# Kernel optimization log

Hardware: AMD Instinct MI355X
Metric: run time of the kernel (lower is better)

Reference implementation:

```python
import jax, jax.numpy as jnp
import numpy as np

N, E = 50000, 800000
IN, H = 128, 128
NTYPE, NSCHOOL, NTIME, NAUTHOR = 20, 30, 15, 200


def setup_inputs() -> dict:
    key = jax.random.key(0)
    ks = jax.random.split(key, 20)

    def lin(k, i, o):  # kaiming-ish init
        return jax.random.normal(k, (i, o), jnp.float32) * (1.0 / np.sqrt(i))

    return {
        "x0": jax.random.normal(ks[0], (N, IN), jnp.float32),
        "edge_index": jax.random.randint(ks[1], (2, E), 0, N, dtype=jnp.int64),
        # GCNConv weights (x @ W + b after aggregation)
        "W1": lin(ks[2], IN, H),   "b1": jnp.zeros((H,), jnp.float32),
        "Wt": lin(ks[3], H, NTYPE),    "bt": jnp.zeros((NTYPE,), jnp.float32),
        "Ws": lin(ks[4], H, NSCHOOL), "bs": jnp.zeros((NSCHOOL,), jnp.float32),
        "Wa": lin(ks[5], H, NAUTHOR), "ba": jnp.zeros((NAUTHOR,), jnp.float32),
        # classification heads (Linear stored as [in, out])
        "Wct": lin(ks[6], NTYPE, NTYPE),       "bct": jnp.zeros((NTYPE,), jnp.float32),
        "Wcs": lin(ks[7], NSCHOOL, NSCHOOL), "bcs": jnp.zeros((NSCHOOL,), jnp.float32),
        "Wtf": lin(ks[8], IN, NTIME),          "btf": jnp.zeros((NTIME,), jnp.float32),
        "Wca": lin(ks[9], NAUTHOR, NAUTHOR), "bca": jnp.zeros((NAUTHOR,), jnp.float32),
    }


def reference(x0, edge_index, W1, b1, Wt, bt, Ws, bs, Wa, ba,
              Wct, bct, Wcs, bcs, Wtf, btf, Wca, bca):
    n = x0.shape[0]
    src, dst = edge_index[0], edge_index[1]
    # GCNConv default: add self-loops, symmetric deg^{-1/2} normalization
    loop = jnp.arange(n, dtype=edge_index.dtype)
    src_f = jnp.concatenate([src, loop])  # [E+N]
    dst_f = jnp.concatenate([dst, loop])
    deg = jax.ops.segment_sum(jnp.ones(src_f.shape[0], jnp.float32), dst_f, num_segments=n)
    dinv = jnp.where(deg > 0, jax.lax.rsqrt(deg), 0.0)
    norm = dinv[src_f] * dinv[dst_f]  # [E+N]

    def conv(x, W, b):
        xt = x @ W                                   # transform first (small out dim)
        msg = xt[src_f] * norm[:, None]              # [E+N, out]
        return jax.ops.segment_sum(msg, dst_f, num_segments=n) + b

    h = jax.nn.relu(conv(x0, W1, b1))  # dropout is identity at inference

    out_type = jax.nn.softmax(conv(h, Wt, bt) @ Wct + bct, axis=-1)
    out_school = jax.nn.softmax(conv(h, Ws, bs) @ Wcs + bcs, axis=-1)
    out_time = jax.nn.softmax(x0 @ Wtf + btf, axis=-1)  # head reads x0 directly
    out_author = jax.nn.softmax(conv(h, Wa, ba) @ Wca + bca, axis=-1)
    return (out_type, out_school, out_time, out_author)
```

## Files before the change

kernel.cpp:

```cpp
#include <hip/hip_runtime.h>
#include <math.h>


typedef short short8 __attribute__((ext_vector_type(8)));
typedef float f32x4 __attribute__((ext_vector_type(4)));

static __device__ __forceinline__ unsigned short f2bf(float x) {
  unsigned u = __float_as_uint(x);
  u += 0x7fff + ((u >> 16) & 1);
  return (unsigned short)(u >> 16);
}
static __device__ __forceinline__ unsigned pack2bf(float lo, float hi) {
  return ((unsigned)f2bf(hi) << 16) | (unsigned)f2bf(lo);
}
static __device__ __forceinline__ float bflo(unsigned u) {
  return __uint_as_float(u << 16);
}
static __device__ __forceinline__ float bfhi(unsigned u) {
  return __uint_as_float(u & 0xffff0000u);
}

__global__ void k_zero(int* __restrict__ p, int n) {
  int i = blockIdx.x * blockDim.x + threadIdx.x;
  if (i < n) p[i] = 0;
}

__global__ void k_deg(const int* __restrict__ dst, int E, int* __restrict__ deg) {
  int e = blockIdx.x * blockDim.x + threadIdx.x;
  if (e < E) atomicAdd(&deg[dst[e]], 1);
}

__global__ void k_scan1(const int* __restrict__ deg, int n,
                        int* __restrict__ excl, int* __restrict__ bsum) {
  __shared__ int sm[256];
  int i = blockIdx.x * 256 + threadIdx.x;
  int v = (i < n) ? deg[i] : 0;
  sm[threadIdx.x] = v;
  __syncthreads();
#pragma unroll
  for (int o = 1; o < 256; o <<= 1) {
    int t = (threadIdx.x >= o) ? sm[threadIdx.x - o] : 0;
    __syncthreads();
    sm[threadIdx.x] += t;
    __syncthreads();
  }
  if (i < n) excl[i] = sm[threadIdx.x] - v;
  if (threadIdx.x == 255) bsum[blockIdx.x] = sm[255];
}

__global__ void k_scan2(int* __restrict__ bsum, int nb) {
  __shared__ int sm[256];
  int v = (threadIdx.x < nb) ? bsum[threadIdx.x] : 0;
  sm[threadIdx.x] = v;
  __syncthreads();
#pragma unroll
  for (int o = 1; o < 256; o <<= 1) {
    int t = (threadIdx.x >= o) ? sm[threadIdx.x - o] : 0;
    __syncthreads();
    sm[threadIdx.x] += t;
    __syncthreads();
  }
  if (threadIdx.x < nb) bsum[threadIdx.x] = sm[threadIdx.x] - v;
}

__global__ void k_finalize(int* __restrict__ row_off, const int* __restrict__ bsum,
                           const int* __restrict__ deg, int* __restrict__ cursor,
                           float* __restrict__ dinv, int n) {
  int i = blockIdx.x * 256 + threadIdx.x;
  if (i < n) {
    int ro = row_off[i] + bsum[blockIdx.x];
    row_off[i] = ro;
    cursor[i] = ro;
    dinv[i] = rsqrtf((float)(deg[i] + 1));
  }
}

__global__ void k_fill(const int* __restrict__ src, const int* __restrict__ dst,
                       int E, int* __restrict__ cursor, int* __restrict__ csr) {
  int e = blockIdx.x * blockDim.x + threadIdx.x;
  if (e < E) {
    int d = dst[e];
    int p = atomicAdd(&cursor[d], 1);
    csr[p] = src[e];
  }
}

__global__ __launch_bounds__(256) void k_scale(
    const float* __restrict__ X, const float* __restrict__ dinv,
    unsigned* __restrict__ Y, int n) {
  int t = blockIdx.x * 256 + threadIdx.x;
  int total = n * 64;
  if (t < total) {
    int row = t >> 6;
    float d = dinv[row];
    float2 v = reinterpret_cast<const float2*>(X)[t];
    Y[t] = pack2bf(v.x * d, v.y * d);
  }
}

__global__ __launch_bounds__(256) void k_agg(
    const unsigned* __restrict__ Y, unsigned* __restrict__ out,
    const int* __restrict__ row_off, const int* __restrict__ deg,
    const int* __restrict__ csr, const float* __restrict__ dinv, int n) {
  int wave = threadIdx.x >> 6;
  int lane = threadIdx.x & 63;
  int i = blockIdx.x * 4 + wave;
  if (i >= n) return;
  int start = row_off[i];
  int cnt = deg[i];
  float ax = 0.f, ay = 0.f;
  int j = 0;
  for (; j + 3 < cnt; j += 4) {
    int s0 = csr[start + j];
    int s1 = csr[start + j + 1];
    int s2 = csr[start + j + 2];
    int s3 = csr[start + j + 3];
    unsigned u0 = Y[(size_t)s0 * 64 + lane];
    unsigned u1 = Y[(size_t)s1 * 64 + lane];
    unsigned u2 = Y[(size_t)s2 * 64 + lane];
    unsigned u3 = Y[(size_t)s3 * 64 + lane];
    ax += (bflo(u0) + bflo(u1)) + (bflo(u2) + bflo(u3));
    ay += (bfhi(u0) + bfhi(u1)) + (bfhi(u2) + bfhi(u3));
  }
  for (; j < cnt; ++j) {
    int s0 = csr[start + j];
    unsigned u0 = Y[(size_t)s0 * 64 + lane];
    ax += bflo(u0);
    ay += bfhi(u0);
  }
  unsigned us = Y[(size_t)i * 64 + lane];
  float di = dinv[i];
  out[(size_t)i * 64 + lane] = pack2bf((ax + bflo(us)) * di, (ay + bfhi(us)) * di);
}

__global__ void k_pack128(const float* __restrict__ W, unsigned short* __restrict__ P) {
  int t = blockIdx.x * 256 + threadIdx.x;
  int i = t >> 7, c = t & 127;
  P[((i >> 3) * 128 + c) * 8 + (i & 7)] = f2bf(W[t]);
}

__global__ void k_fuse(const float* __restrict__ Wt, const float* __restrict__ bt,
                       const float* __restrict__ Wct, const float* __restrict__ bct,
                       const float* __restrict__ Ws, const float* __restrict__ bs,
                       const float* __restrict__ Wcs, const float* __restrict__ bcs,
                       const float* __restrict__ Wa, const float* __restrict__ ba,
                       const float* __restrict__ Wca, const float* __restrict__ bca,
                       unsigned short* __restrict__ WfPk, float* __restrict__ bf) {
  int c = blockIdx.x;
  int i = threadIdx.x;
  float acc = 0.f, bacc = 0.f;
  if (c < 20) {
    for (int k = 0; k < 20; ++k) {
      float w2 = Wct[k * 20 + c];
      acc += Wt[i * 20 + k] * w2;
      bacc += bt[k] * w2;
    }
    bacc += bct[c];
  } else if (c < 50) {
    int cc = c - 20;
    for (int k = 0; k < 30; ++k) {
      float w2 = Wcs[k * 30 + cc];
      acc += Ws[i * 30 + k] * w2;
      bacc += bs[k] * w2;
    }
    bacc += bcs[cc];
  } else if (c < 250) {
    int cc = c - 50;
    for (int k = 0; k < 200; ++k) {
      float w2 = Wca[k * 200 + cc];
      acc += Wa[i * 200 + k] * w2;
      bacc += ba[k] * w2;
    }
    bacc += bca[cc];
  }
  WfPk[((i >> 3) * 256 + c) * 8 + (i & 7)] = f2bf(acc);
  if (i == 0) bf[c] = bacc;
}

__global__ __launch_bounds__(256) void k_mfma_gemm128(
    const short* __restrict__ A, const unsigned short* __restrict__ Wpk,
    const float* __restrict__ bias, const float* __restrict__ dinv,
    unsigned short* __restrict__ out, int n) {
  int wave = threadIdx.x >> 6, lane = threadIdx.x & 63;
  int lr = lane & 15, lg = lane >> 4;
  int r0 = blockIdx.x * 64 + wave * 16;
  if (r0 >= n) return;
  int ar = r0 + lr;
  if (ar >= n) ar = n - 1;
  const short* Arow = A + (size_t)ar * 128;
  short8 afr[4];
#pragma unroll
  for (int kk = 0; kk < 4; ++kk)
    afr[kk] = *reinterpret_cast<const short8*>(Arow + kk * 32 + lg * 8);
  f32x4 acc[8];
#pragma unroll
  for (int t = 0; t < 8; ++t) acc[t] = (f32x4){0.f, 0.f, 0.f, 0.f};
  const short8* Wp8 = reinterpret_cast<const short8*>(Wpk);
#pragma unroll
  for (int t = 0; t < 8; ++t) {
#pragma unroll
    for (int kk = 0; kk < 4; ++kk) {
      short8 bfr = Wp8[(kk * 4 + lg) * 128 + t * 16 + lr];
      acc[t] = __builtin_amdgcn_mfma_f32_16x16x32_bf16(afr[kk], bfr, acc[t], 0, 0, 0);
    }
  }
  int rloc = r0 + lg * 4;
#pragma unroll
  for (int t = 0; t < 8; ++t) {
    int col = t * 16 + lr;
    float b = bias[col];
#pragma unroll
    for (int reg = 0; reg < 4; ++reg) {
      int row = rloc + reg;
      if (row < n) {
        float v = fmaxf(acc[t][reg] + b, 0.f) * dinv[row];
        out[(size_t)row * 128 + col] = f2bf(v);
      }
    }
  }
}

__global__ __launch_bounds__(256) void k_heads_fused(
    const short* __restrict__ A, const unsigned short* __restrict__ Wpk,
    const float* __restrict__ bf, float* __restrict__ outT,
    float* __restrict__ outS, float* __restrict__ outA, int n) {
  int wave = threadIdx.x >> 6, lane = threadIdx.x & 63;
  int lr = lane & 15, lg = lane >> 4;
  int r0 = blockIdx.x * 64 + wave * 16;
  if (r0 >= n) return;
  int ar = r0 + lr;
  if (ar >= n) ar = n - 1;
  const short* Arow = A + (size_t)ar * 128;
  short8 afr[4];
#pragma unroll
  for (int kk = 0; kk < 4; ++kk)
    afr[kk] = *reinterpret_cast<const short8*>(Arow + kk * 32 + lg * 8);
  f32x4 acc[16];
#pragma unroll
  for (int t = 0; t < 16; ++t) acc[t] = (f32x4){0.f, 0.f, 0.f, 0.f};
  const short8* Wp8 = reinterpret_cast<const short8*>(Wpk);
#pragma unroll
  for (int t = 0; t < 16; ++t) {
#pragma unroll
    for (int kk = 0; kk < 4; ++kk) {
      short8 bfr = Wp8[(kk * 4 + lg) * 256 + t * 16 + lr];
      acc[t] = __builtin_amdgcn_mfma_f32_16x16x32_bf16(afr[kk], bfr, acc[t], 0, 0, 0);
    }
  }
  float bias_l[16];
#pragma unroll
  for (int t = 0; t < 16; ++t) bias_l[t] = bf[t * 16 + lr];
  int rloc = r0 + lg * 4;
#pragma unroll
  for (int reg = 0; reg < 4; ++reg) {
    int row = rloc + reg;
    float v[16];
    float mT = -INFINITY, mS = -INFINITY, mA = -INFINITY;
#pragma unroll
    for (int t = 0; t < 16; ++t) {
      v[t] = acc[t][reg] + bias_l[t];
      int c = t * 16 + lr;
      if (c < 20) mT = fmaxf(mT, v[t]);
      else if (c < 50) mS = fmaxf(mS, v[t]);
      else if (c < 250) mA = fmaxf(mA, v[t]);
    }
#pragma unroll
    for (int o = 8; o; o >>= 1) {
      mT = fmaxf(mT, __shfl_xor(mT, o, 64));
      mS = fmaxf(mS, __shfl_xor(mS, o, 64));
      mA = fmaxf(mA, __shfl_xor(mA, o, 64));
    }
    float sT = 0.f, sS = 0.f, sA = 0.f;
#pragma unroll
    for (int t = 0; t < 16; ++t) {
      int c = t * 16 + lr;
      float m = (c < 20) ? mT : (c < 50) ? mS : mA;
      float ex = __expf(v[t] - m);
      v[t] = ex;
      if (c < 20) sT += ex;
      else if (c < 50) sS += ex;
      else if (c < 250) sA += ex;
    }
#pragma unroll
    for (int o = 8; o; o >>= 1) {
      sT += __shfl_xor(sT, o, 64);
      sS += __shfl_xor(sS, o, 64);
      sA += __shfl_xor(sA, o, 64);
    }
    float iT = 1.f / sT, iS = 1.f / sS, iA = 1.f / sA;
    if (row < n) {
#pragma unroll
      for (int t = 0; t < 16; ++t) {
        int c = t * 16 + lr;
        if (c < 20) outT[(size_t)row * 20 + c] = v[t] * iT;
        else if (c < 50) outS[(size_t)row * 30 + (c - 20)] = v[t] * iS;
        else if (c < 250) outA[(size_t)row * 200 + (c - 50)] = v[t] * iA;
      }
    }
  }
}

__global__ __launch_bounds__(256) void k_time(
    const float* __restrict__ x0, const float* __restrict__ Wtf,
    const float* __restrict__ btf, float* __restrict__ outT, int n) {
  __shared__ float sW[128][16];
  __shared__ float sb[16];
  for (int t = threadIdx.x; t < 128 * 16; t += 256) {
    int k = t >> 4, j = t & 15;
    sW[k][j] = (j < 15) ? Wtf[k * 15 + j] : 0.f;
  }
  if (threadIdx.x < 16) sb[threadIdx.x] = (threadIdx.x < 15) ? btf[threadIdx.x] : 0.f;
  __syncthreads();
  int j = threadIdx.x & 15;
  int rl = threadIdx.x >> 4;
  int r = blockIdx.x * 16 + rl;
  if (r >= n) return;
  float acc = sb[j];
  const float4* xr = reinterpret_cast<const float4*>(x0 + (size_t)r * 128);
  for (int k4 = 0; k4 < 32; ++k4) {
    float4 xv = xr[k4];
    acc += xv.x * sW[k4 * 4 + 0][j] + xv.y * sW[k4 * 4 + 1][j] +
           xv.z * sW[k4 * 4 + 2][j] + xv.w * sW[k4 * 4 + 3][j];
  }
  float m = (j < 15) ? acc : -INFINITY;
#pragma unroll
  for (int o = 8; o; o >>= 1) m = fmaxf(m, __shfl_xor(m, o, 16));
  float e = (j < 15) ? __expf(acc - m) : 0.f;
  float s = e;
#pragma unroll
  for (int o = 8; o; o >>= 1) s += __shfl_xor(s, o, 16);
  if (j < 15) outT[(size_t)r * 15 + j] = e / s;
}

extern "C" void kernel_launch(void* const* d_in, const int* in_sizes, int n_in,
                              void* d_out, int out_size, void* d_ws, size_t ws_size,
                              hipStream_t stream) {
  const float* x0 = (const float*)d_in[0];
  const int* ei = (const int*)d_in[1];
  const float* W1 = (const float*)d_in[2];
  const float* b1 = (const float*)d_in[3];
  const float* Wt = (const float*)d_in[4];
  const float* bt = (const float*)d_in[5];
  const float* Ws = (const float*)d_in[6];
  const float* bs = (const float*)d_in[7];
  const float* Wa = (const float*)d_in[8];
  const float* ba = (const float*)d_in[9];
  const float* Wct = (const float*)d_in[10];
  const float* bct = (const float*)d_in[11];
  const float* Wcs = (const float*)d_in[12];
  const float* bcs = (const float*)d_in[13];
  const float* Wtf = (const float*)d_in[14];
  const float* btf = (const float*)d_in[15];
  const float* Wca = (const float*)d_in[16];
  const float* bca = (const float*)d_in[17];
  (void)n_in; (void)out_size; (void)ws_size;

  int N = in_sizes[0] / 128;
  int E = in_sizes[1] / 2;
  float* out = (float*)d_out;

  char* ws = (char*)d_ws;
  size_t off = 0;
  auto alloc = [&](size_t bytes) -> void* {
    void* p = ws + off;
    off = (off + bytes + 255) & ~(size_t)255;
    return p;
  };
  int* deg = (int*)alloc((size_t)N * 4);
  int* row_off = (int*)alloc((size_t)N * 4);
  int* bsum = (int*)alloc(256 * 4);
  int* cursor = (int*)alloc((size_t)N * 4);
  float* dinv = (float*)alloc((size_t)N * 4);
  int* csr = (int*)alloc((size_t)E * 4);
  unsigned short* WfPk = (unsigned short*)alloc((size_t)128 * 256 * 2);
  unsigned short* W1Pk = (unsigned short*)alloc((size_t)128 * 128 * 2);
  float* bf = (float*)alloc(256 * 4);
  unsigned* Yb = (unsigned*)alloc((size_t)N * 64 * 4);
  unsigned* Ab = (unsigned*)alloc((size_t)N * 64 * 4);
  unsigned* Bb = (unsigned*)alloc((size_t)N * 64 * 4);

  const int* srcp = ei;
  const int* dstp = ei + E;
  int gE = (E + 255) / 256;
  int gN = (N + 255) / 256;

  k_zero<<<gN, 256, 0, stream>>>(deg, N);
  k_deg<<<gE, 256, 0, stream>>>(dstp, E, deg);
  k_scan1<<<gN, 256, 0, stream>>>(deg, N, row_off, bsum);
  k_scan2<<<1, 256, 0, stream>>>(bsum, gN);
  k_finalize<<<gN, 256, 0, stream>>>(row_off, bsum, deg, cursor, dinv, N);
  k_fill<<<gE, 256, 0, stream>>>(srcp, dstp, E, cursor, csr);
  k_pack128<<<64, 256, 0, stream>>>(W1, W1Pk);
  k_fuse<<<256, 128, 0, stream>>>(Wt, bt, Wct, bct, Ws, bs, Wcs, bcs, Wa, ba, Wca,
                                  bca, WfPk, bf);
  k_scale<<<(N * 64 + 255) / 256, 256, 0, stream>>>(x0, dinv, Yb, N);
  k_agg<<<(N + 3) / 4, 256, 0, stream>>>(Yb, Ab, row_off, deg, csr, dinv, N);
  k_mfma_gemm128<<<(N + 63) / 64, 256, 0, stream>>>(
      (const short*)Ab, W1Pk, b1, dinv, (unsigned short*)Bb, N);
  k_agg<<<(N + 3) / 4, 256, 0, stream>>>(Bb, Ab, row_off, deg, csr, dinv, N);
  k_heads_fused<<<(N + 63) / 64, 256, 0, stream>>>(
      (const short*)Ab, WfPk, bf, out, out + (size_t)N * 20, out + (size_t)N * 65, N);
  k_time<<<(N + 15) / 16, 256, 0, stream>>>(x0, Wtf, btf, out + (size_t)N * 50, N);
}
```

Measured before the change: 381.6 us.

## Split GEMM and heads columns across wave pairs with LDS-staged A tiles

Both MFMA kernels now handle 32 rows per block. The A tile is staged through shared memory, and each pair of waves splits the output columns between them, so twice as many blocks launch and each wave holds half the accumulators. In the fused heads kernel the author softmax spans both column halves, so row max and row sum are exchanged through LDS with extra barriers. This aims to raise occupancy and parallelism, at the cost of more blocks, extra syncs, and each block reading the weight matrix for its share of the columns.

```diff
diff --git a/kernel.cpp b/kernel.cpp
--- a/kernel.cpp
+++ b/kernel.cpp
@@ -177,37 +177,49 @@
   if (i == 0) bf[c] = bacc;
 }
 
+static __device__ __forceinline__ void stage32(
+    const short* __restrict__ A, short (*sAb)[136], int rowBase, int n, int tid) {
+  for (int t = tid; t < 32 * 16; t += 256) {
+    int r = t >> 4, c8 = t & 15;
+    int gr = rowBase + r;
+    short8 v = (short8){0, 0, 0, 0, 0, 0, 0, 0};
+    if (gr < n) v = *reinterpret_cast<const short8*>(A + (size_t)gr * 128 + c8 * 8);
+    *reinterpret_cast<short8*>(&sAb[r][c8 * 8]) = v;
+  }
+}
+
 __global__ __launch_bounds__(256) void k_mfma_gemm128(
     const short* __restrict__ A, const unsigned short* __restrict__ Wpk,
     const float* __restrict__ bias, const float* __restrict__ dinv,
     unsigned short* __restrict__ out, int n) {
+  __shared__ short sAb[32][136];
+  int rowBase = blockIdx.x * 32;
+  stage32(A, sAb, rowBase, n, threadIdx.x);
+  __syncthreads();
   int wave = threadIdx.x >> 6, lane = threadIdx.x & 63;
+  int rg = wave >> 1, ch = wave & 1;
   int lr = lane & 15, lg = lane >> 4;
-  int r0 = blockIdx.x * 64 + wave * 16;
-  if (r0 >= n) return;
-  int ar = r0 + lr;
-  if (ar >= n) ar = n - 1;
-  const short* Arow = A + (size_t)ar * 128;
+  int r0 = rowBase + rg * 16;
   short8 afr[4];
 #pragma unroll
   for (int kk = 0; kk < 4; ++kk)
-    afr[kk] = *reinterpret_cast<const short8*>(Arow + kk * 32 + lg * 8);
-  f32x4 acc[8];
-#pragma unroll
-  for (int t = 0; t < 8; ++t) acc[t] = (f32x4){0.f, 0.f, 0.f, 0.f};
+    afr[kk] = *reinterpret_cast<const short8*>(&sAb[rg * 16 + lr][kk * 32 + lg * 8]);
+  f32x4 acc[4];
+#pragma unroll
+  for (int t = 0; t < 4; ++t) acc[t] = (f32x4){0.f, 0.f, 0.f, 0.f};
   const short8* Wp8 = reinterpret_cast<const short8*>(Wpk);
 #pragma unroll
-  for (int t = 0; t < 8; ++t) {
+  for (int t = 0; t < 4; ++t) {
 #pragma unroll
     for (int kk = 0; kk < 4; ++kk) {
-      short8 bfr = Wp8[(kk * 4 + lg) * 128 + t * 16 + lr];
+      short8 bfr = Wp8[(kk * 4 + lg) * 128 + ch * 64 + t * 16 + lr];
       acc[t] = __builtin_amdgcn_mfma_f32_16x16x32_bf16(afr[kk], bfr, acc[t], 0, 0, 0);
     }
   }
   int rloc = r0 + lg * 4;
 #pragma unroll
-  for (int t = 0; t < 8; ++t) {
-    int col = t * 16 + lr;
+  for (int t = 0; t < 4; ++t) {
+    int col = ch * 64 + t * 16 + lr;
     float b = bias[col];
 #pragma unroll
     for (int reg = 0; reg < 4; ++reg) {
@@ -224,45 +236,48 @@
     const short* __restrict__ A, const unsigned short* __restrict__ Wpk,
     const float* __restrict__ bf, float* __restrict__ outT,
     float* __restrict__ outS, float* __restrict__ outA, int n) {
+  __shared__ short sAb[32][136];
+  __shared__ float aM[2][2][16];
+  __shared__ float aS[2][2][16];
+  int rowBase = blockIdx.x * 32;
+  stage32(A, sAb, rowBase, n, threadIdx.x);
+  __syncthreads();
   int wave = threadIdx.x >> 6, lane = threadIdx.x & 63;
+  int rg = wave >> 1, ch = wave & 1;
   int lr = lane & 15, lg = lane >> 4;
-  int r0 = blockIdx.x * 64 + wave * 16;
-  if (r0 >= n) return;
-  int ar = r0 + lr;
-  if (ar >= n) ar = n - 1;
-  const short* Arow = A + (size_t)ar * 128;
+  int r0 = rowBase + rg * 16;
+  int cb = ch * 128;
   short8 afr[4];
 #pragma unroll
   for (int kk = 0; kk < 4; ++kk)
-    afr[kk] = *reinterpret_cast<const short8*>(Arow + kk * 32 + lg * 8);
-  f32x4 acc[16];
-#pragma unroll
-  for (int t = 0; t < 16; ++t) acc[t] = (f32x4){0.f, 0.f, 0.f, 0.f};
+    afr[kk] = *reinterpret_cast<const short8*>(&sAb[rg * 16 + lr][kk * 32 + lg * 8]);
+  f32x4 acc[8];
+#pragma unroll
+  for (int t = 0; t < 8; ++t) acc[t] = (f32x4){0.f, 0.f, 0.f, 0.f};
   const short8* Wp8 = reinterpret_cast<const short8*>(Wpk);
 #pragma unroll
-  for (int t = 0; t < 16; ++t) {
+  for (int t = 0; t < 8; ++t) {
 #pragma unroll
     for (int kk = 0; kk < 4; ++kk) {
-      short8 bfr = Wp8[(kk * 4 + lg) * 256 + t * 16 + lr];
+      short8 bfr = Wp8[(kk * 4 + lg) * 256 + cb + t * 16 + lr];
       acc[t] = __builtin_amdgcn_mfma_f32_16x16x32_bf16(afr[kk], bfr, acc[t], 0, 0, 0);
     }
   }
-  float bias_l[16];
-#pragma unroll
-  for (int t = 0; t < 16; ++t) bias_l[t] = bf[t * 16 + lr];
-  int rloc = r0 + lg * 4;
+  float bias_l[8];
+#pragma unroll
+  for (int t = 0; t < 8; ++t) bias_l[t] = bf[cb + t * 16 + lr];
+  float mTr[4], mSr[4], mAr[4];
 #pragma unroll
   for (int reg = 0; reg < 4; ++reg) {
-    int row = rloc + reg;
-    float v[16];
     float mT = -INFINITY, mS = -INFINITY, mA = -INFINITY;
 #pragma unroll
-    for (int t = 0; t < 16; ++t) {
-      v[t] = acc[t][reg] + bias_l[t];
-      int c = t * 16 + lr;
-      if (c < 20) mT = fmaxf(mT, v[t]);
-      else if (c < 50) mS = fmaxf(mS, v[t]);
-      else if (c < 250) mA = fmaxf(mA, v[t]);
+    for (int t = 0; t < 8; ++t) {
+      int c = cb + t * 16 + lr;
+      float val = acc[t][reg] + bias_l[t];
+      acc[t][reg] = val;
+      if (c < 20) mT = fmaxf(mT, val);
+      else if (c < 50) mS = fmaxf(mS, val);
+      else if (c < 250) mA = fmaxf(mA, val);
     }
 #pragma unroll
     for (int o = 8; o; o >>= 1) {
@@ -270,16 +285,26 @@
       mS = fmaxf(mS, __shfl_xor(mS, o, 64));
       mA = fmaxf(mA, __shfl_xor(mA, o, 64));
     }
+    mTr[reg] = mT; mSr[reg] = mS; mAr[reg] = mA;
+    if (lr == 0) aM[rg][ch][lg * 4 + reg] = mA;
+  }
+  __syncthreads();
+#pragma unroll
+  for (int reg = 0; reg < 4; ++reg)
+    mAr[reg] = fmaxf(mAr[reg], aM[rg][ch ^ 1][lg * 4 + reg]);
+  float sTr[4], sSr[4], sAr[4];
+#pragma unroll
+  for (int reg = 0; reg < 4; ++reg) {
     float sT = 0.f, sS = 0.f, sA = 0.f;
 #pragma unroll
-    for (int t = 0; t < 16; ++t) {
-      int c = t * 16 + lr;
-      float m = (c < 20) ? mT : (c < 50) ? mS : mA;
-      float ex = __expf(v[t] - m);
-      v[t] = ex;
-      if (c < 20) sT += ex;
-      else if (c < 50) sS += ex;
-      else if (c < 250) sA += ex;
+    for (int t = 0; t < 8; ++t) {
+      int c = cb + t * 16 + lr;
+      float m = (c < 20) ? mTr[reg] : (c < 50) ? mSr[reg] : mAr[reg];
+      float e = __expf(acc[t][reg] - m);
+      acc[t][reg] = e;
+      if (c < 20) sT += e;
+      else if (c < 50) sS += e;
+      else if (c < 250) sA += e;
     }
 #pragma unroll
     for (int o = 8; o; o >>= 1) {
@@ -287,15 +312,26 @@
       sS += __shfl_xor(sS, o, 64);
       sA += __shfl_xor(sA, o, 64);
     }
-    float iT = 1.f / sT, iS = 1.f / sS, iA = 1.f / sA;
-    if (row < n) {
-#pragma unroll
-      for (int t = 0; t < 16; ++t) {
-        int c = t * 16 + lr;
-        if (c < 20) outT[(size_t)row * 20 + c] = v[t] * iT;
-        else if (c < 50) outS[(size_t)row * 30 + (c - 20)] = v[t] * iS;
-        else if (c < 250) outA[(size_t)row * 200 + (c - 50)] = v[t] * iA;
-      }
+    sTr[reg] = sT; sSr[reg] = sS; sAr[reg] = sA;
+    if (lr == 0) aS[rg][ch][lg * 4 + reg] = sA;
+  }
+  __syncthreads();
+#pragma unroll
+  for (int reg = 0; reg < 4; ++reg)
+    sAr[reg] += aS[rg][ch ^ 1][lg * 4 + reg];
+  int rloc = r0 + lg * 4;
+#pragma unroll
+  for (int reg = 0; reg < 4; ++reg) {
+    int row = rloc + reg;
+    if (row >= n) continue;
+    float iT = 1.f / sTr[reg], iS = 1.f / sSr[reg], iA = 1.f / sAr[reg];
+#pragma unroll
+    for (int t = 0; t < 8; ++t) {
+      int c = cb + t * 16 + lr;
+      float e = acc[t][reg];
+      if (c < 20) outT[(size_t)row * 20 + c] = e * iT;
+      else if (c < 50) outS[(size_t)row * 30 + (c - 20)] = e * iS;
+      else if (c < 250) outA[(size_t)row * 200 + (c - 50)] = e * iA;
     }
   }
 }
@@ -383,6 +419,7 @@
   const int* dstp = ei + E;
   int gE = (E + 255) / 256;
   int gN = (N + 255) / 256;
+  int g32 = (N + 31) / 32;
 
   k_zero<<<gN, 256, 0, stream>>>(deg, N);
   k_deg<<<gE, 256, 0, stream>>>(dstp, E, deg);
@@ -395,10 +432,10 @@
                                   bca, WfPk, bf);
   k_scale<<<(N * 64 + 255) / 256, 256, 0, stream>>>(x0, dinv, Yb, N);
   k_agg<<<(N + 3) / 4, 256, 0, stream>>>(Yb, Ab, row_off, deg, csr, dinv, N);
-  k_mfma_gemm128<<<(N + 63) / 64, 256, 0, stream>>>(
+  k_mfma_gemm128<<<g32, 256, 0, stream>>>(
       (const short*)Ab, W1Pk, b1, dinv, (unsigned short*)Bb, N);
   k_agg<<<(N + 3) / 4, 256, 0, stream>>>(Bb, Ab, row_off, deg, csr, dinv, N);
-  k_heads_fused<<<(N + 63) / 64, 256, 0, stream>>>(
+  k_heads_fused<<<g32, 256, 0, stream>>>(
       (const short*)Ab, WfPk, bf, out, out + (size_t)N * 20, out + (size_t)N * 65, N);
   k_time<<<(N + 15) / 16, 256, 0, stream>>>(x0, Wtf, btf, out + (size_t)N * 50, N);
 }
```

New measurement: 351.7 us. 1.08x faster.
